# Kernel optimization log

Hardware: AMD Instinct MI355X
Metric: run time of the kernel (lower is better)

Reference implementation:

```python
import jax, jax.numpy as jnp
import numpy as np

B, C, H, W = 8, 256, 128, 128
NH, WS = 8, 8
HD = C // NH
WNH, WNW = H // WS, W // WS


def _rel_pos_index():
    coords = np.stack(np.meshgrid(np.arange(WS), np.arange(WS), indexing='ij'))  # [2,ws,ws]
    flat = coords.reshape(2, -1)
    rel = (flat[:, :, None] - flat[:, None, :]).transpose(1, 2, 0)  # [ws^2,ws^2,2]
    rel[..., 0] += WS - 1
    rel[..., 1] += WS - 1
    rel[..., 0] *= 2 * WS - 1
    return jnp.asarray(rel.sum(-1))  # [ws^2,ws^2]


def grid_sample(img, grid):
    # Bilinear, padding_mode='zeros', align_corners=True. img [N,C,H,W], grid [N,Hg,Wg,2] (x,y in [-1,1])
    N, Ci, Hi, Wi = img.shape
    gx = (grid[..., 0] + 1.0) * 0.5 * (Wi - 1)
    gy = (grid[..., 1] + 1.0) * 0.5 * (Hi - 1)
    x0 = jnp.floor(gx)
    y0 = jnp.floor(gy)
    x0i = x0.astype(jnp.int32)
    y0i = y0.astype(jnp.int32)
    wx1 = gx - x0
    wx0 = 1.0 - wx1
    wy1 = gy - y0
    wy0 = 1.0 - wy1
    nb = jnp.arange(N)[:, None, None]

    def corner(yi, xi, wgt):
        valid = (yi >= 0) & (yi < Hi) & (xi >= 0) & (xi < Wi)
        yc = jnp.clip(yi, 0, Hi - 1)
        xc = jnp.clip(xi, 0, Wi - 1)
        val = img[nb, :, yc, xc]  # [N,Hg,Wg,C]
        return val * (wgt * valid)[..., None]

    out = (corner(y0i, x0i, wy0 * wx0) + corner(y0i, x0i + 1, wy0 * wx1)
           + corner(y0i + 1, x0i, wy1 * wx0) + corner(y0i + 1, x0i + 1, wy1 * wx1))
    return jnp.transpose(out, (0, 3, 1, 2))


def setup_inputs() -> dict:
    key = jax.random.key(0)
    ks = jax.random.split(key, 10)
    f = lambda k, s, sc=1.0: jax.random.normal(k, s, dtype=jnp.float32) * sc
    return {
        'x': f(ks[0], (B, C, H, W)),
        'qkv_w': f(ks[1], (3 * C, C), 0.02),
        'qkv_b': f(ks[2], (3 * C,), 0.02),
        'bias_w': f(ks[3], (2 * NH, C), 0.02),
        'bias_b': f(ks[4], (2 * NH,), 0.02),
        'scale_w': f(ks[5], (2 * NH, C), 0.02),
        'scale_b': f(ks[6], (2 * NH,), 0.02),
        'proj_w': f(ks[7], (C, C), 0.02),
        'proj_b': f(ks[8], (C,), 0.02),
        'rpb_table': f(ks[9], ((2 * WS - 1) ** 2, NH), 0.02),
    }


def reference(x, qkv_w, qkv_b, bias_w, bias_b, scale_w, scale_b, proj_w, proj_b, rpb_table):
    scale = HD ** -0.5
    N = B * NH
    # ---- deterministic base sampling coordinates (shift=0, no padding since H,W % WS == 0) ----
    lin_w = jnp.linspace(-1.0, 1.0, W)
    lin_h = jnp.linspace(-1.0, 1.0, H)
    winref_w = lin_w.reshape(WNW, WS).mean(-1)  # window centers along width
    winref_h = lin_h.reshape(WNH, WS).mean(-1)
    off_w = jnp.arange(WS) * 2.0 / (W - 1)
    off_w = off_w - off_w.mean()
    off_h = jnp.arange(WS) * 2.0 / (H - 1)
    off_h = off_h - off_h.mean()
    base_x = jnp.broadcast_to(winref_w[None, None, :, None] + off_w[None, None, None, :], (WNH, WS, WNW, WS))
    base_y = jnp.broadcast_to((winref_h[:, None] + off_h[None, :])[:, :, None, None], (WNH, WS, WNW, WS))
    # ---- predicted per-head per-window biases & scales ----
    xp = jax.nn.leaky_relu(x.reshape(B, C, WNH, WS, WNW, WS).mean((3, 5)))  # [B,C,WNH,WNW]
    biases = (jnp.einsum('oc,bchw->bohw', bias_w, xp) + bias_b[None, :, None, None]).reshape(N, 2, WNH, WNW)
    bx = biases[:, 0] / WNW  # sampling_biases[:,0] / (w // ws)
    by = biases[:, 1] / WNH
    scales = (jnp.einsum('oc,bchw->bohw', scale_w, xp) + scale_b[None, :, None, None]).reshape(N, 2, WNH, WNW)
    sx, sy = scales[:, 0], scales[:, 1]
    # final = base + local_offsets * scale + bias (broadcast [N,WNH,1,WNW,1] over window interior)
    cx = base_x[None] + off_w[None, None, None, None, :] * sx[:, :, None, :, None] + bx[:, :, None, :, None]
    cy = base_y[None] + off_h[None, None, :, None, None] * sy[:, :, None, :, None] + by[:, :, None, :, None]
    grid = jnp.stack([cx, cy], -1).reshape(N, H, W, 2)
    # ---- qkv via 1x1 conv ----
    qkv = (jnp.einsum('oc,bchw->bohw', qkv_w, x) + qkv_b[None, :, None, None]).reshape(B, 3, NH, HD, H, W)
    q = qkv[:, 0].reshape(N, HD, H, W)
    k = qkv[:, 1].reshape(N, HD, H, W)
    v = qkv[:, 2].reshape(N, HD, H, W)
    ksamp = grid_sample(k, grid)
    vsamp = grid_sample(v, grid)

    def win(t):  # [N,HD,H,W] -> [B, nWin, NH, WS*WS, HD]
        t = t.reshape(B, NH, HD, WNH, WS, WNW, WS)
        return jnp.transpose(t, (0, 3, 5, 1, 4, 6, 2)).reshape(B, WNH * WNW, NH, WS * WS, HD)

    qw, kw, vw = win(q), win(ksamp), win(vsamp)
    rpb = jnp.transpose(rpb_table[_rel_pos_index().reshape(-1)].reshape(WS * WS, WS * WS, NH), (2, 0, 1))
    attn = jnp.einsum('bwhqd,bwhkd->bwhqk', qw, kw) * scale + rpb[None, None]
    attn = jax.nn.softmax(attn, axis=-1)
    out = jnp.einsum('bwhqk,bwhkd->bwhqd', attn, vw)
    out = out.reshape(B, WNH, WNW, NH, WS, WS, HD)
    out = jnp.transpose(out, (0, 3, 6, 1, 4, 2, 5)).reshape(B, C, H, W)
    out = jnp.einsum('oc,bchw->bohw', proj_w, out) + proj_b[None, :, None, None]
    return out
```

## Files before the change

kernel.cpp:

```cpp
#include <hip/hip_runtime.h>
#include <hip/hip_fp16.h>

#define B_ 8
#define C_ 256
#define H_ 128
#define W_ 128
#define NH_ 8
#define WS_ 8
#define HD_ 32
#define WN_ 16
#define NWIN_ 256
#define HW_ 16384

typedef unsigned short ushort_t;
typedef unsigned int uint_t;
typedef __attribute__((ext_vector_type(8))) short short8;
typedef _Float16 __attribute__((ext_vector_type(8))) half8;
typedef __attribute__((ext_vector_type(4))) float f32x4;

__device__ __forceinline__ ushort_t bf16_rtn(float x) {
    uint_t u = __float_as_uint(x);
    return (ushort_t)((u + 0x7FFFu + ((u >> 16) & 1u)) >> 16);
}
__device__ __forceinline__ uint_t bfpack(float a, float b) {
    return (uint_t)bf16_rtn(a) | ((uint_t)bf16_rtn(b) << 16);
}
__device__ __forceinline__ uint_t h2pack(float a, float b) {
    __half2 h = __floats2half2_rn(a, b);
    return __builtin_bit_cast(uint_t, h);
}

__global__ __launch_bounds__(256) void wpack_kernel(const float* __restrict__ w,
                            ushort_t* __restrict__ wpk) {
    int u = blockIdx.x*256 + threadIdx.x;
    int lane = u & 63;
    int f    = (u >> 6) & 3;
    int kk   = (u >> 8) & 1;
    int ks   = (u >> 9) & 3;
    int wm   = (u >> 11) & 1;
    int oc   = u >> 12;
    int o = oc*128 + wm*64 + f*16 + (lane & 15);
    int c = ks*64 + kk*32 + (lane >> 4)*8;
    const float* src = w + (size_t)o*256 + c;
    float4 v0 = *(const float4*)src;
    float4 v1 = *(const float4*)(src + 4);
    uint4 Hv;
    Hv.x = h2pack(v0.x, v0.y); Hv.y = h2pack(v0.z, v0.w);
    Hv.z = h2pack(v1.x, v1.y); Hv.w = h2pack(v1.z, v1.w);
    ((uint4*)wpk)[u] = Hv;
}

__global__ __launch_bounds__(256) void wconv_kernel(const float* __restrict__ w,
                            ushort_t* __restrict__ wh, int n4) {
    int i = blockIdx.x*256 + threadIdx.x;
    if (i >= n4) return;
    float4 v = ((const float4*)w)[i];
    ((uint2*)wh)[i] = make_uint2(bfpack(v.x, v.y), bfpack(v.z, v.w));
}

__global__ __launch_bounds__(256) void rpb_expand_kernel(const float* __restrict__ rpb_table,
                            float* __restrict__ rpbT) {
    int nh = blockIdx.x;
    int t = threadIdx.x;
    #pragma unroll
    for (int rr = 0; rr < 16; ++rr) {
        int e = t*16 + rr;
        int kcol = e >> 6, qrow = e & 63;
        int yq = qrow >> 3, xq = qrow & 7, yk = kcol >> 3, xk = kcol & 7;
        int idx = (yq - yk + 7)*15 + (xq - xk + 7);
        rpbT[((size_t)nh*64 + kcol)*64 + qrow] = rpb_table[idx*8 + nh];
    }
}

__global__ __launch_bounds__(256) void pool2_kernel(const float* __restrict__ xpart, float* __restrict__ xp) {
    int bc = blockIdx.x;
    int t = threadIdx.x;
    int wy = t >> 4, wxg = t & 15;
    const float* src = xpart + (size_t)bc*2048;
    float s = 0.f;
    #pragma unroll
    for (int i = 0; i < 8; ++i) s += src[(wy*8+i)*16 + wxg];
    s *= (1.f/64.f);
    xp[(size_t)bc*256 + t] = s > 0.f ? s : 0.01f*s;
}

__global__ __launch_bounds__(256) void params_kernel(const float* __restrict__ xp,
                              const float* __restrict__ bias_w, const float* __restrict__ bias_b,
                              const float* __restrict__ scale_w, const float* __restrict__ scale_b,
                              float* __restrict__ params) {
    __shared__ float xs[256];
    int blk = blockIdx.x;
    int b = blk >> 8, win = blk & 255;
    int t = threadIdx.x;
    xs[t] = xp[((size_t)(b*256 + t))*256 + win];
    __syncthreads();
    if (t < 32) {
        int which = t >> 4;
        int o = t & 15;
        const float* Wm = which ? scale_w : bias_w;
        float acc = which ? scale_b[o] : bias_b[o];
        for (int c = 0; c < 256; ++c) acc += Wm[o*256 + c] * xs[c];
        int nh = o >> 1, comp = o & 1;
        int n = b*8 + nh;
        float v = which ? acc : 3.96875f * acc;
        params[((size_t)(n*256 + win))*4 + which*2 + comp] = v;
    }
}

__global__ __launch_bounds__(256) void mgemm_qkvf_kernel(const ushort_t* __restrict__ wpk,
                            const float* __restrict__ x,
                            const float* __restrict__ bias,
                            ushort_t* __restrict__ qt, ushort_t* __restrict__ kv,
                            float* __restrict__ xpart) {
    __shared__ __align__(16) float Btile[64*129];
    int bid = blockIdx.x;
    int orig = (bid & 7) * 384 + (bid >> 3);
    int ocg = orig % 3;
    int rest = orig / 3;
    int hrow = rest & 127;
    int zb = rest >> 7;
    int p0 = hrow * 128;
    const float* xb = x + (size_t)zb*C_*HW_;
    ushort_t* qtb = qt + (size_t)zb*HW_*256;
    ushort_t* kvb = kv + (size_t)zb*8*HW_*64;
    int t = threadIdx.x;
    int lane = t & 63, wid = t >> 6;
    int wm = wid >> 1, wn = wid & 1;
    int qi = lane >> 4, rl = lane & 15;

    const ushort_t* wpkA0 = wpk + (size_t)((ocg*2 + 0)*2 + wm)*16384;
    const ushort_t* wpkA1 = wpk + (size_t)((ocg*2 + 1)*2 + wm)*16384;

    f32x4 acc[2][4][4];
    #pragma unroll
    for (int o2 = 0; o2 < 2; ++o2)
        #pragma unroll
        for (int f = 0; f < 4; ++f)
            #pragma unroll
            for (int g = 0; g < 4; ++g)
                acc[o2][f][g] = (f32x4){0.f, 0.f, 0.f, 0.f};

    for (int ks = 0; ks < 4; ++ks) {
        int c0 = ks*64;
        __syncthreads();
        #pragma unroll
        for (int r = 0; r < 8; ++r) {
            int task = t + r*256;
            int cl = task >> 5, p4 = (task & 31)*4;
            float4 v = *(const float4*)(xb + (size_t)(c0+cl)*HW_ + p0 + p4);
            float* dst = &Btile[cl*129 + p4];
            dst[0]=v.x; dst[1]=v.y; dst[2]=v.z; dst[3]=v.w;
        }
        __syncthreads();
        if (ocg == 0) {
            #pragma unroll
            for (int r = 0; r < 4; ++r) {
                int task = t + r*256;
                int cl = task >> 4, wxg = task & 15;
                float s = 0.f;
                #pragma unroll
                for (int j = 0; j < 8; ++j) s += Btile[cl*129 + wxg*8 + j];
                xpart[(((size_t)zb*256 + c0+cl)*128 + hrow)*16 + wxg] = s;
            }
        }
        #pragma unroll
        for (int kk = 0; kk < 2; ++kk) {
            half8 bfh[4];
            #pragma unroll
            for (int g = 0; g < 4; ++g) {
                int pix = wn*64 + g*16 + rl;
                const float* col = &Btile[(kk*32 + qi*8)*129 + pix];
                float f0 = col[0*129], f1 = col[1*129], f2 = col[2*129], f3 = col[3*129];
                float f4 = col[4*129], f5 = col[5*129], f6 = col[6*129], f7 = col[7*129];
                uint4 bu;
                bu.x = h2pack(f0, f1); bu.y = h2pack(f2, f3);
                bu.z = h2pack(f4, f5); bu.w = h2pack(f6, f7);
                bfh[g] = __builtin_bit_cast(half8, bu);
            }
            int wkoff = ((ks*2 + kk)*4)*512 + lane*8;
            {
                half8 afh[4];
                const ushort_t* wk = wpkA0 + wkoff;
                #pragma unroll
                for (int f = 0; f < 4; ++f)
                    afh[f] = *(const half8*)(wk + f*512);
                #pragma unroll
                for (int f = 0; f < 4; ++f)
                    #pragma unroll
                    for (int g = 0; g < 4; ++g)
                        acc[0][f][g] = __builtin_amdgcn_mfma_f32_16x16x32_f16(afh[f], bfh[g], acc[0][f][g], 0, 0, 0);
            }
            {
                half8 afh[4];
                const ushort_t* wk = wpkA1 + wkoff;
                #pragma unroll
                for (int f = 0; f < 4; ++f)
                    afh[f] = *(const half8*)(wk + f*512);
                #pragma unroll
                for (int f = 0; f < 4; ++f)
                    #pragma unroll
                    for (int g = 0; g < 4; ++g)
                        acc[1][f][g] = __builtin_amdgcn_mfma_f32_16x16x32_f16(afh[f], bfh[g], acc[1][f][g], 0, 0, 0);
            }
        }
    }

    float* tb = Btile;
    #pragma unroll
    for (int o2 = 0; o2 < 2; ++o2) {
        int o0 = ocg*256 + o2*128;
        #pragma unroll
        for (int pm = 0; pm < 2; ++pm) {
            #pragma unroll
            for (int pn = 0; pn < 2; ++pn) {
                __syncthreads();
                if (wm == pm && wn == pn) {
                    #pragma unroll
                    for (int f = 0; f < 4; ++f)
                        #pragma unroll
                        for (int g = 0; g < 4; ++g)
                            #pragma unroll
                            for (int r = 0; r < 4; ++r)
                                tb[(f*16 + qi*4 + r)*67 + g*16 + rl] = acc[o2][f][g][r];
                }
                __syncthreads();
                {
                    int pxl = t >> 2, cg = t & 3;
                    size_t pix = p0 + pn*64 + pxl;
                    int obase = o0 + pm*64 + cg*16;
                    int type = obase >> 8;
                    int oo = obase & 255;
                    int head = oo >> 5;
                    ushort_t* dst = (type == 0)
                        ? qtb + pix*256 + oo
                        : kvb + ((size_t)head*HW_ + pix)*64 + ((type == 2) ? 32 : 0) + (oo & 31);
                    float v[16];
                    #pragma unroll
                    for (int e = 0; e < 16; ++e) v[e] = tb[(cg*16 + e)*67 + pxl];
                    float4 b0 = *(const float4*)&bias[obase];
                    float4 b1 = *(const float4*)&bias[obase + 4];
                    float4 b2 = *(const float4*)&bias[obase + 8];
                    float4 b3 = *(const float4*)&bias[obase + 12];
                    uint4 H0, H1;
                    H0.x = h2pack(v[0]+b0.x,  v[1]+b0.y);  H0.y = h2pack(v[2]+b0.z,  v[3]+b0.w);
                    H0.z = h2pack(v[4]+b1.x,  v[5]+b1.y);  H0.w = h2pack(v[6]+b1.z,  v[7]+b1.w);
                    H1.x = h2pack(v[8]+b2.x,  v[9]+b2.y);  H1.y = h2pack(v[10]+b2.z, v[11]+b2.w);
                    H1.z = h2pack(v[12]+b3.x, v[13]+b3.y); H1.w = h2pack(v[14]+b3.z, v[15]+b3.w);
                    *(uint4*)dst = H0;
                    *(uint4*)(dst + 8) = H1;
                }
            }
        }
    }
}

__global__ __launch_bounds__(256) void mgemm_proj_kernel(const ushort_t* __restrict__ wp,
                            const ushort_t* __restrict__ at,
                            const float* __restrict__ bias, float* __restrict__ out) {
    __shared__ __align__(16) uint4 smem[2048];
    uint4* Ah = smem; uint4* Bh = smem + 1024;
    int bid = blockIdx.x;
    int orig = (bid & 7) * 256 + (bid >> 3);
    int o0 = (orig % 2) * 128;
    int rest = orig / 2;
    int p0 = (rest & 127) * 128;
    int zb = rest >> 7;
    const ushort_t* xh = at + (size_t)zb*HW_*256;
    float* outb = out + (size_t)zb*C_*HW_;
    int t = threadIdx.x;
    int lane = t & 63, wid = t >> 6;
    int wm = wid >> 1, wn = wid & 1;
    int q = lane >> 4, rl = lane & 15;

    f32x4 acc[4][4];
    #pragma unroll
    for (int f = 0; f < 4; ++f)
        #pragma unroll
        for (int g = 0; g < 4; ++g)
            acc[f][g] = (f32x4){0.f, 0.f, 0.f, 0.f};

    int srow = t >> 1, shalf = t & 1;
    int sw = srow & 7;

    for (int ks = 0; ks < 4; ++ks) {
        int c0 = ks * 64;
        __syncthreads();
        {
            const uint4* a_h = (const uint4*)(wp + (size_t)(o0+srow)*256 + c0);
            const uint4* b_h = (const uint4*)(xh + (size_t)(p0+srow)*256 + c0);
            #pragma unroll
            for (int jj = 0; jj < 4; ++jj) {
                int u = shalf*4 + jj;
                int d = srow*8 + (u ^ sw);
                Ah[d] = a_h[u]; Bh[d] = b_h[u];
            }
        }
        __syncthreads();
        #pragma unroll
        for (int kk = 0; kk < 2; ++kk) {
            short8 afh[4], bfh[4];
            #pragma unroll
            for (int f = 0; f < 4; ++f) {
                int row = wm*64 + f*16 + rl;
                int u = (kk*4 + q) ^ (row & 7);
                afh[f] = __builtin_bit_cast(short8, Ah[row*8 + u]);
            }
            #pragma unroll
            for (int g = 0; g < 4; ++g) {
                int row = wn*64 + g*16 + rl;
                int u = (kk*4 + q) ^ (row & 7);
                bfh[g] = __builtin_bit_cast(short8, Bh[row*8 + u]);
            }
            #pragma unroll
            for (int f = 0; f < 4; ++f)
                #pragma unroll
                for (int g = 0; g < 4; ++g)
                    acc[f][g] = __builtin_amdgcn_mfma_f32_16x16x32_bf16(afh[f], bfh[g], acc[f][g], 0, 0, 0);
        }
    }
    #pragma unroll
    for (int f = 0; f < 4; ++f) {
        float4 bb = *(const float4*)&bias[o0 + wm*64 + f*16 + q*4];
        float bbv[4] = {bb.x, bb.y, bb.z, bb.w};
        #pragma unroll
        for (int g = 0; g < 4; ++g) {
            int p = p0 + wn*64 + g*16 + rl;
            #pragma unroll
            for (int r = 0; r < 4; ++r) {
                int o = o0 + wm*64 + f*16 + q*4 + r;
                outb[(size_t)o*HW_ + p] = acc[f][g][r] + bbv[r];
            }
        }
    }
}

__global__ __launch_bounds__(256) void attn_kernel(const ushort_t* __restrict__ qt,
                            const ushort_t* __restrict__ kv,
                            const float* __restrict__ params_,
                            const float* __restrict__ rpbT,
                            ushort_t* __restrict__ at) {
    __shared__ __align__(16) ushort_t smem[64*40 + 64*40 + 32*72 + 64*40];
    ushort_t (*Q_lds)[40]   = (ushort_t(*)[40])smem;
    ushort_t (*K_lds)[40]   = (ushort_t(*)[40])(smem + 2560);
    ushort_t (*VT_lds)[72]  = (ushort_t(*)[72])(smem + 5120);
    ushort_t (*P_lds)[72]   = (ushort_t(*)[72])smem;
    ushort_t (*OUT_lds)[40] = (ushort_t(*)[40])(smem + 5120 + 2304);

    int b = blockIdx.y;
    int blk = blockIdx.x;
    int win = blk >> 3, nh = blk & 7;
    int wy = win >> 4, wx = win & 15;
    int t = threadIdx.x;
    int lane = t & 63, wid = t >> 6;

    const float* pp = params_ + ((size_t)((b*8 + nh)*256 + win))*4;
    float ox = pp[0], oy = pp[1], sx = pp[2], sy = pp[3];

    const ushort_t* qtb = qt + (size_t)b*HW_*256;
    const ushort_t* kvb = kv + ((size_t)(b*8 + nh))*HW_*64;
    ushort_t* ath = at + (size_t)b*HW_*256;

    {
        int tok = t >> 2, cg = t & 3;
        int i = tok >> 3, j = tok & 7;
        size_t pix = (size_t)(wy*8 + i)*W_ + wx*8 + j;
        *(uint4*)&Q_lds[tok][cg*8] = *(const uint4*)(qtb + pix*256 + nh*32 + cg*8);
    }
    {
        int tokq = lane >> 3, sub = lane & 7;
        #pragma unroll
        for (int r = 0; r < 2; ++r) {
            int tok = wid*16 + r*8 + tokq;
            int i = tok >> 3, j = tok & 7;
            int h = wy*8 + i, wpx = wx*8 + j;
            float gx = (float)wpx + ((float)j - 3.5f)*sx + ox;
            float gy = (float)h  + ((float)i - 3.5f)*sy + oy;
            float x0f = floorf(gx), y0f = floorf(gy);
            int x0 = (int)x0f, y0 = (int)y0f;
            float wx1 = gx - x0f, wy1 = gy - y0f;
            float wxz = 1.f - wx1, wyz = 1.f - wy1;
            int x1 = x0 + 1, y1 = y0 + 1;
            float m00 = wyz*wxz * ((y0>=0 && y0<H_ && x0>=0 && x0<W_) ? 1.f : 0.f);
            float m01 = wyz*wx1 * ((y0>=0 && y0<H_ && x1>=0 && x1<W_) ? 1.f : 0.f);
            float m10 = wy1*wxz * ((y1>=0 && y1<H_ && x0>=0 && x0<W_) ? 1.f : 0.f);
            float m11 = wy1*wx1 * ((y1>=0 && y1<H_ && x1>=0 && x1<W_) ? 1.f : 0.f);
            int x0c = min(max(x0,0),W_-1), x1c = min(max(x1,0),W_-1);
            int y0c = min(max(y0,0),H_-1), y1c = min(max(y1,0),H_-1);
            size_t p00 = (size_t)y0c*W_ + x0c, p01 = (size_t)y0c*W_ + x1c;
            size_t p10 = (size_t)y1c*W_ + x0c, p11 = (size_t)y1c*W_ + x1c;
            __half2 a0 = __float2half2_rn(0.f), a1 = a0, a2 = a0, a3 = a0;
            #define CORNER(PIX, M) { \
                uint4 u = *(const uint4*)(kvb + (PIX)*64 + sub*8); \
                __half2 wv = __float2half2_rn(M); \
                a0 = __hfma2(__builtin_bit_cast(__half2, u.x), wv, a0); \
                a1 = __hfma2(__builtin_bit_cast(__half2, u.y), wv, a1); \
                a2 = __hfma2(__builtin_bit_cast(__half2, u.z), wv, a2); \
                a3 = __hfma2(__builtin_bit_cast(__half2, u.w), wv, a3); }
            CORNER(p00, m00)
            CORNER(p01, m01)
            CORNER(p10, m10)
            CORNER(p11, m11)
            #undef CORNER
            if (sub < 4) {
                uint4 Kv;
                Kv.x = __builtin_bit_cast(uint_t, a0); Kv.y = __builtin_bit_cast(uint_t, a1);
                Kv.z = __builtin_bit_cast(uint_t, a2); Kv.w = __builtin_bit_cast(uint_t, a3);
                *(uint4*)&K_lds[tok][sub*8] = Kv;
            } else {
                int d0 = (sub - 4)*8;
                VT_lds[d0+0][tok] = __half_as_ushort(__low2half(a0));
                VT_lds[d0+1][tok] = __half_as_ushort(__high2half(a0));
                VT_lds[d0+2][tok] = __half_as_ushort(__low2half(a1));
                VT_lds[d0+3][tok] = __half_as_ushort(__high2half(a1));
                VT_lds[d0+4][tok] = __half_as_ushort(__low2half(a2));
                VT_lds[d0+5][tok] = __half_as_ushort(__high2half(a2));
                VT_lds[d0+6][tok] = __half_as_ushort(__low2half(a3));
                VT_lds[d0+7][tok] = __half_as_ushort(__high2half(a3));
            }
        }
    }
    __syncthreads();

    int q = lane >> 4, rl = lane & 15;
    const float scale = 0.17677669529663687f;

    half8 a_frag = *(const half8*)&Q_lds[wid*16 + rl][q*8];
    half8 b_frag[4];
    #pragma unroll
    for (int g = 0; g < 4; ++g)
        b_frag[g] = *(const half8*)&K_lds[g*16 + rl][q*8];
    __syncthreads();

    f32x4 accS[4];
    #pragma unroll
    for (int g = 0; g < 4; ++g)
        accS[g] = __builtin_amdgcn_mfma_f32_16x16x32_f16(a_frag, b_frag[g], (f32x4){0.f,0.f,0.f,0.f}, 0, 0, 0);

    float Sv[4][4];
    const float* rpbb = rpbT + (size_t)nh*4096;
    int m0 = wid*16 + q*4;
    #pragma unroll
    for (int g = 0; g < 4; ++g) {
        float4 rv = *(const float4*)&rpbb[(g*16 + rl)*64 + m0];
        Sv[g][0] = accS[g][0]*scale + rv.x;
        Sv[g][1] = accS[g][1]*scale + rv.y;
        Sv[g][2] = accS[g][2]*scale + rv.z;
        Sv[g][3] = accS[g][3]*scale + rv.w;
    }
    float inv[4];
    #pragma unroll
    for (int r = 0; r < 4; ++r) {
        float pm = fmaxf(fmaxf(Sv[0][r], Sv[1][r]), fmaxf(Sv[2][r], Sv[3][r]));
        pm = fmaxf(pm, __shfl_xor(pm, 1));
        pm = fmaxf(pm, __shfl_xor(pm, 2));
        pm = fmaxf(pm, __shfl_xor(pm, 4));
        pm = fmaxf(pm, __shfl_xor(pm, 8));
        float s = 0.f;
        #pragma unroll
        for (int g = 0; g < 4; ++g) {
            float e = __expf(Sv[g][r] - pm);
            Sv[g][r] = e;
            s += e;
        }
        s += __shfl_xor(s, 1);
        s += __shfl_xor(s, 2);
        s += __shfl_xor(s, 4);
        s += __shfl_xor(s, 8);
        inv[r] = 1.f / s;
    }
    #pragma unroll
    for (int r = 0; r < 4; ++r) {
        int m = wid*16 + q*4 + r;
        #pragma unroll
        for (int g = 0; g < 4; ++g)
            P_lds[m][g*16 + rl] = __half_as_ushort(__float2half(Sv[g][r]*inv[r]));
    }

    f32x4 accO[2] = {(f32x4){0.f,0.f,0.f,0.f}, (f32x4){0.f,0.f,0.f,0.f}};
    #pragma unroll
    for (int ks = 0; ks < 2; ++ks) {
        half8 p_frag = *(const half8*)&P_lds[wid*16 + rl][ks*32 + q*8];
        #pragma unroll
        for (int g2 = 0; g2 < 2; ++g2) {
            half8 v_frag = *(const half8*)&VT_lds[g2*16 + rl][ks*32 + q*8];
            accO[g2] = __builtin_amdgcn_mfma_f32_16x16x32_f16(p_frag, v_frag, accO[g2], 0, 0, 0);
        }
    }
    #pragma unroll
    for (int r = 0; r < 4; ++r) {
        int m = wid*16 + q*4 + r;
        OUT_lds[m][rl]      = bf16_rtn(accO[0][r]);
        OUT_lds[m][16 + rl] = bf16_rtn(accO[1][r]);
    }
    __syncthreads();
    {
        int tok = t >> 2, cg = t & 3;
        int i2 = tok >> 3, j2 = tok & 7;
        size_t pix = (size_t)(wy*8 + i2)*W_ + wx*8 + j2;
        *(uint4*)(ath + pix*256 + nh*32 + cg*8) = *(const uint4*)&OUT_lds[tok][cg*8];
    }
}

extern "C" void kernel_launch(void* const* d_in, const int* in_sizes, int n_in,
                              void* d_out, int out_size, void* d_ws, size_t ws_size,
                              hipStream_t stream) {
    const float* x       = (const float*)d_in[0];
    const float* qkv_w   = (const float*)d_in[1];
    const float* qkv_b   = (const float*)d_in[2];
    const float* bias_w  = (const float*)d_in[3];
    const float* bias_b  = (const float*)d_in[4];
    const float* scale_w = (const float*)d_in[5];
    const float* scale_b = (const float*)d_in[6];
    const float* proj_w  = (const float*)d_in[7];
    const float* proj_b  = (const float*)d_in[8];
    const float* rpb     = (const float*)d_in[9];
    float* out = (float*)d_out;

    char* ws = (char*)d_ws;
    float*    xp       = (float*)ws;     ws += (size_t)524288*4;
    float*    params   = (float*)ws;     ws += (size_t)65536*4;
    float*    xpart    = (float*)ws;     ws += (size_t)4194304*4;
    float*    rpbT     = (float*)ws;     ws += (size_t)8*4096*4;
    ushort_t* wpk      = (ushort_t*)ws;  ws += (size_t)768*256*2;
    ushort_t* wp       = (ushort_t*)ws;  ws += (size_t)256*256*2;
    ushort_t* at       = (ushort_t*)ws;  ws += (size_t)B_*HW_*256*2;
    ushort_t* qt       = (ushort_t*)ws;  ws += (size_t)B_*HW_*256*2;
    ushort_t* kv       = (ushort_t*)ws;

    wpack_kernel<<<dim3(96), 256, 0, stream>>>(qkv_w, wpk);
    wconv_kernel<<<dim3(64), 256, 0, stream>>>(proj_w, wp, 256*256/4);
    rpb_expand_kernel<<<dim3(NH_), 256, 0, stream>>>(rpb, rpbT);
    mgemm_qkvf_kernel<<<dim3(3072), 256, 0, stream>>>(wpk, x, qkv_b, qt, kv, xpart);
    pool2_kernel <<<dim3(B_*C_), 256, 0, stream>>>(xpart, xp);
    params_kernel<<<dim3(B_*NWIN_), 256, 0, stream>>>(xp, bias_w, bias_b, scale_w, scale_b, params);
    attn_kernel<<<dim3(NH_*NWIN_, B_), 256, 0, stream>>>(qt, kv, params, rpbT, at);
    mgemm_proj_kernel<<<dim3(2048), 256, 0, stream>>>(wp, at, proj_b, out);
}
```

Measured before the change: 322.3 us.

## Merge prep kernels and restage QKV epilogue through one fp16 shared tile

The three small weight and rpb preparation kernels are merged into a single launch that branches on block index. The QKV GEMM epilogue used to stage fp32 accumulators through shared memory in four serialized per-warp passes, each with two barriers. It now adds the bias in registers, converts to fp16, writes the whole 128x128 tile to a padded ushort shared buffer in one pass, and then stores 16-byte runs to the output. This removes launch overhead and most epilogue barriers, at the cost of scalar 16-bit shared-memory reads and possible bank conflicts in the gather phase.

```diff
diff --git a/kernel.cpp b/kernel.cpp
--- a/kernel.cpp
+++ b/kernel.cpp
@@ -30,45 +30,43 @@
     return __builtin_bit_cast(uint_t, h);
 }
 
-__global__ __launch_bounds__(256) void wpack_kernel(const float* __restrict__ w,
-                            ushort_t* __restrict__ wpk) {
-    int u = blockIdx.x*256 + threadIdx.x;
-    int lane = u & 63;
-    int f    = (u >> 6) & 3;
-    int kk   = (u >> 8) & 1;
-    int ks   = (u >> 9) & 3;
-    int wm   = (u >> 11) & 1;
-    int oc   = u >> 12;
-    int o = oc*128 + wm*64 + f*16 + (lane & 15);
-    int c = ks*64 + kk*32 + (lane >> 4)*8;
-    const float* src = w + (size_t)o*256 + c;
-    float4 v0 = *(const float4*)src;
-    float4 v1 = *(const float4*)(src + 4);
-    uint4 Hv;
-    Hv.x = h2pack(v0.x, v0.y); Hv.y = h2pack(v0.z, v0.w);
-    Hv.z = h2pack(v1.x, v1.y); Hv.w = h2pack(v1.z, v1.w);
-    ((uint4*)wpk)[u] = Hv;
-}
-
-__global__ __launch_bounds__(256) void wconv_kernel(const float* __restrict__ w,
-                            ushort_t* __restrict__ wh, int n4) {
-    int i = blockIdx.x*256 + threadIdx.x;
-    if (i >= n4) return;
-    float4 v = ((const float4*)w)[i];
-    ((uint2*)wh)[i] = make_uint2(bfpack(v.x, v.y), bfpack(v.z, v.w));
-}
-
-__global__ __launch_bounds__(256) void rpb_expand_kernel(const float* __restrict__ rpb_table,
-                            float* __restrict__ rpbT) {
-    int nh = blockIdx.x;
+__global__ __launch_bounds__(256) void prep_kernel(const float* __restrict__ qkv_w,
+                            ushort_t* __restrict__ wpk,
+                            const float* __restrict__ proj_w, ushort_t* __restrict__ wp,
+                            const float* __restrict__ rpb_table, float* __restrict__ rpbT) {
+    int blk = blockIdx.x;
     int t = threadIdx.x;
-    #pragma unroll
-    for (int rr = 0; rr < 16; ++rr) {
-        int e = t*16 + rr;
-        int kcol = e >> 6, qrow = e & 63;
-        int yq = qrow >> 3, xq = qrow & 7, yk = kcol >> 3, xk = kcol & 7;
-        int idx = (yq - yk + 7)*15 + (xq - xk + 7);
-        rpbT[((size_t)nh*64 + kcol)*64 + qrow] = rpb_table[idx*8 + nh];
+    if (blk < 96) {
+        int u = blk*256 + t;
+        int lane = u & 63;
+        int f    = (u >> 6) & 3;
+        int kk   = (u >> 8) & 1;
+        int ks   = (u >> 9) & 3;
+        int wm   = (u >> 11) & 1;
+        int oc   = u >> 12;
+        int o = oc*128 + wm*64 + f*16 + (lane & 15);
+        int c = ks*64 + kk*32 + (lane >> 4)*8;
+        const float* src = qkv_w + (size_t)o*256 + c;
+        float4 v0 = *(const float4*)src;
+        float4 v1 = *(const float4*)(src + 4);
+        uint4 Hv;
+        Hv.x = h2pack(v0.x, v0.y); Hv.y = h2pack(v0.z, v0.w);
+        Hv.z = h2pack(v1.x, v1.y); Hv.w = h2pack(v1.z, v1.w);
+        ((uint4*)wpk)[u] = Hv;
+    } else if (blk < 160) {
+        int i = (blk - 96)*256 + t;
+        float4 v = ((const float4*)proj_w)[i];
+        ((uint2*)wp)[i] = make_uint2(bfpack(v.x, v.y), bfpack(v.z, v.w));
+    } else {
+        int nh = blk - 160;
+        #pragma unroll
+        for (int rr = 0; rr < 16; ++rr) {
+            int e = t*16 + rr;
+            int kcol = e >> 6, qrow = e & 63;
+            int yq = qrow >> 3, xq = qrow & 7, yk = kcol >> 3, xk = kcol & 7;
+            int idx = (yq - yk + 7)*15 + (xq - xk + 7);
+            rpbT[((size_t)nh*64 + kcol)*64 + qrow] = rpb_table[idx*8 + nh];
+        }
     }
 }
 
@@ -112,7 +110,9 @@
                             const float* __restrict__ bias,
                             ushort_t* __restrict__ qt, ushort_t* __restrict__ kv,
                             float* __restrict__ xpart) {
-    __shared__ __align__(16) float Btile[64*129];
+    __shared__ __align__(16) char smemraw[33280];
+    float* Btile = (float*)smemraw;
+    ushort_t (*OutT)[130] = (ushort_t(*)[130])smemraw;
     int bid = blockIdx.x;
     int orig = (bid & 7) * 384 + (bid >> 3);
     int ocg = orig % 3;
@@ -205,50 +205,47 @@
         }
     }
 
-    float* tb = Btile;
     #pragma unroll
     for (int o2 = 0; o2 < 2; ++o2) {
         int o0 = ocg*256 + o2*128;
-        #pragma unroll
-        for (int pm = 0; pm < 2; ++pm) {
-            #pragma unroll
-            for (int pn = 0; pn < 2; ++pn) {
-                __syncthreads();
-                if (wm == pm && wn == pn) {
-                    #pragma unroll
-                    for (int f = 0; f < 4; ++f)
-                        #pragma unroll
-                        for (int g = 0; g < 4; ++g)
-                            #pragma unroll
-                            for (int r = 0; r < 4; ++r)
-                                tb[(f*16 + qi*4 + r)*67 + g*16 + rl] = acc[o2][f][g][r];
+        __syncthreads();
+        #pragma unroll
+        for (int f = 0; f < 4; ++f) {
+            float4 bb = *(const float4*)&bias[o0 + wm*64 + f*16 + qi*4];
+            float bbv[4] = {bb.x, bb.y, bb.z, bb.w};
+            #pragma unroll
+            for (int g = 0; g < 4; ++g) {
+                int px = wn*64 + g*16 + rl;
+                #pragma unroll
+                for (int r = 0; r < 4; ++r) {
+                    int ol = wm*64 + f*16 + qi*4 + r;
+                    OutT[ol][px] = __half_as_ushort(__float2half(acc[o2][f][g][r] + bbv[r]));
                 }
-                __syncthreads();
-                {
-                    int pxl = t >> 2, cg = t & 3;
-                    size_t pix = p0 + pn*64 + pxl;
-                    int obase = o0 + pm*64 + cg*16;
-                    int type = obase >> 8;
-                    int oo = obase & 255;
-                    int head = oo >> 5;
-                    ushort_t* dst = (type == 0)
-                        ? qtb + pix*256 + oo
-                        : kvb + ((size_t)head*HW_ + pix)*64 + ((type == 2) ? 32 : 0) + (oo & 31);
-                    float v[16];
-                    #pragma unroll
-                    for (int e = 0; e < 16; ++e) v[e] = tb[(cg*16 + e)*67 + pxl];
-                    float4 b0 = *(const float4*)&bias[obase];
-                    float4 b1 = *(const float4*)&bias[obase + 4];
-                    float4 b2 = *(const float4*)&bias[obase + 8];
-                    float4 b3 = *(const float4*)&bias[obase + 12];
-                    uint4 H0, H1;
-                    H0.x = h2pack(v[0]+b0.x,  v[1]+b0.y);  H0.y = h2pack(v[2]+b0.z,  v[3]+b0.w);
-                    H0.z = h2pack(v[4]+b1.x,  v[5]+b1.y);  H0.w = h2pack(v[6]+b1.z,  v[7]+b1.w);
-                    H1.x = h2pack(v[8]+b2.x,  v[9]+b2.y);  H1.y = h2pack(v[10]+b2.z, v[11]+b2.w);
-                    H1.z = h2pack(v[12]+b3.x, v[13]+b3.y); H1.w = h2pack(v[14]+b3.z, v[15]+b3.w);
-                    *(uint4*)dst = H0;
-                    *(uint4*)(dst + 8) = H1;
-                }
+            }
+        }
+        __syncthreads();
+        {
+            int run = t & 15, prow = t >> 4;
+            int obase = o0 + run*8;
+            int type = obase >> 8;
+            int oo = obase & 255;
+            int head = oo >> 5;
+            #pragma unroll
+            for (int it = 0; it < 8; ++it) {
+                int pxl = it*16 + prow;
+                size_t pix = p0 + pxl;
+                ushort_t hv[8];
+                #pragma unroll
+                for (int e = 0; e < 8; ++e) hv[e] = OutT[run*8 + e][pxl];
+                uint4 Hv;
+                Hv.x = (uint_t)hv[0] | ((uint_t)hv[1]<<16);
+                Hv.y = (uint_t)hv[2] | ((uint_t)hv[3]<<16);
+                Hv.z = (uint_t)hv[4] | ((uint_t)hv[5]<<16);
+                Hv.w = (uint_t)hv[6] | ((uint_t)hv[7]<<16);
+                ushort_t* dst = (type == 0)
+                    ? qtb + pix*256 + oo
+                    : kvb + ((size_t)head*HW_ + pix)*64 + ((type == 2) ? 32 : 0) + (oo & 31);
+                *(uint4*)dst = Hv;
             }
         }
     }
@@ -527,9 +524,7 @@
     ushort_t* qt       = (ushort_t*)ws;  ws += (size_t)B_*HW_*256*2;
     ushort_t* kv       = (ushort_t*)ws;
 
-    wpack_kernel<<<dim3(96), 256, 0, stream>>>(qkv_w, wpk);
-    wconv_kernel<<<dim3(64), 256, 0, stream>>>(proj_w, wp, 256*256/4);
-    rpb_expand_kernel<<<dim3(NH_), 256, 0, stream>>>(rpb, rpbT);
+    prep_kernel<<<dim3(168), 256, 0, stream>>>(qkv_w, wpk, proj_w, wp, rpb, rpbT);
     mgemm_qkvf_kernel<<<dim3(3072), 256, 0, stream>>>(wpk, x, qkv_b, qt, kv, xpart);
     pool2_kernel <<<dim3(B_*C_), 256, 0, stream>>>(xpart, xp);
     params_kernel<<<dim3(B_*NWIN_), 256, 0, stream>>>(xp, bias_w, bias_b, scale_w, scale_b, params);
```

Measured after the change: 368.1 us. 1.14x slower.
